# Optimization experiments

Measured on AMD Instinct MI355X. Metric: run time of the kernel, lower is better.

The kernel has to match this reference:

```python
import jax, jax.numpy as jnp
import numpy as np

LOCAL_RANGE = 7  # module default local_range
NUM_HEADS = 8


def setup_inputs() -> dict:
    key = jax.random.key(0)
    k1, k2, k3 = jax.random.split(key, 3)
    B, S, D = 2, 2048, 512
    hidden_states = jax.random.normal(k1, (B, S, D), dtype=jnp.float32)
    scale = 1.0 / (D ** 0.5)
    Wq = jax.random.normal(k2, (D, D), dtype=jnp.float32) * scale
    Wk = jax.random.normal(k3, (D, D), dtype=jnp.float32) * scale
    return {"hidden_states": hidden_states, "Wq": Wq, "Wk": Wk}


def reference(hidden_states, Wq, Wk):
    B, S, D = hidden_states.shape
    H = NUM_HEADS
    dh = D // H
    # inner attention: only attn_weights matter (context_layer is overwritten)
    q = (hidden_states @ Wq).reshape(B, S, H, dh).transpose(0, 2, 1, 3)  # [B,H,S,dh]
    k = (hidden_states @ Wk).reshape(B, S, H, dh).transpose(0, 2, 1, 3)  # [B,H,S,dh]
    scores = jnp.einsum('bhid,bhjd->bhij', q, k) / (dh ** 0.5)          # [B,H,S,S]
    attn_weights = jax.nn.softmax(scores, axis=-1)
    # band-diagonal local mask: |i-j| <= local_range (vectorized form of the python loop)
    idx = jnp.arange(S)
    band = (jnp.abs(idx[:, None] - idx[None, :]) <= LOCAL_RANGE).astype(attn_weights.dtype)  # [S,S]
    local_w = attn_weights * band
    local_w = local_w / (jnp.sum(local_w, axis=-1, keepdims=True) + 1e-6)
    # context = matmul(local_attn_weights, hidden_states): per-head contraction
    context = jnp.einsum('bhij,bjd->bhid', local_w, hidden_states)       # [B,H,S,D]
    return context
```

## Files before the change

kernel.cpp:

```cpp
#include <hip/hip_runtime.h>
#include <hip/hip_bf16.h>
#include <math.h>

#define SEQ   2048
#define DIM   512
#define NH    8
#define DH    64
#define LR    7

typedef __bf16 bf16_t;
typedef __bf16 bf16x8 __attribute__((ext_vector_type(8)));
typedef float  f32x4  __attribute__((ext_vector_type(4)));

typedef __attribute__((address_space(3))) void  lds_void;
typedef __attribute__((address_space(1))) const void gbl_cvoid;

__global__ __launch_bounds__(256) void prep(
    const float* __restrict__ hs,
    const float* __restrict__ Wq, const float* __restrict__ Wk,
    bf16_t* __restrict__ hsb,
    bf16_t* __restrict__ Wt)
{
    const int tid = threadIdx.x;
    const int bx  = blockIdx.x;

    if (bx < 1024) {
        const size_t base = ((size_t)bx * 256 + tid) * 8;
        const float4 f0 = *(const float4*)(hs + base);
        const float4 f1 = *(const float4*)(hs + base + 4);
        union { bf16_t b[8]; uint4 u; } cv;
        cv.b[0]=(bf16_t)f0.x; cv.b[1]=(bf16_t)f0.y; cv.b[2]=(bf16_t)f0.z; cv.b[3]=(bf16_t)f0.w;
        cv.b[4]=(bf16_t)f1.x; cv.b[5]=(bf16_t)f1.y; cv.b[6]=(bf16_t)f1.z; cv.b[7]=(bf16_t)f1.w;
        *(uint4*)(hsb + base) = cv.u;
        return;
    }

    __shared__ float tile[64][68];
    const int t  = bx - 1024;
    const int k0 = (t & 7) * 64;
    const int n0 = (t >> 3) * 64;
    const float* W = (n0 < DIM) ? Wq : Wk;
    const int nn0 = n0 & (DIM - 1);

    #pragma unroll
    for (int ph = 0; ph < 4; ++ph) {
        const int kk = ph * 16 + (tid >> 4);
        const int nn = (tid & 15) * 4;
        const float4 v = *(const float4*)(W + (size_t)(k0 + kk) * DIM + nn0 + nn);
        tile[kk][nn + 0] = v.x; tile[kk][nn + 1] = v.y;
        tile[kk][nn + 2] = v.z; tile[kk][nn + 3] = v.w;
    }
    __syncthreads();
    #pragma unroll
    for (int ph = 0; ph < 4; ++ph) {
        const int nn = ph * 16 + (tid >> 4);
        const int kk = (tid & 15) * 4;
        union { bf16_t b[4]; ushort4 u; } cv;
        #pragma unroll
        for (int u = 0; u < 4; ++u) cv.b[u] = (bf16_t)tile[kk + u][nn];
        *(ushort4*)(Wt + (size_t)(n0 + nn) * DIM + k0 + kk) = cv.u;
    }
}

__global__ __launch_bounds__(256) void qk_gemm_mfma(
    const bf16_t* __restrict__ A,
    const bf16_t* __restrict__ Bt,
    float* __restrict__ C)
{
    __shared__ bf16_t As[64][32];
    __shared__ bf16_t Bs[128][32];

    const int tid  = threadIdx.x;
    const int wave = tid >> 6;
    const int lane = tid & 63;
    const int l15  = lane & 15;
    const int quad = lane >> 4;
    const int wm   = (wave >> 1) * 32;
    const int wn   = (wave & 1) * 64;
    const int m0   = blockIdx.x * 64;
    const int n0   = blockIdx.y * 128;

    const int srow = lane >> 2;
    const int scol = (lane & 3) * 8;

    const bf16_t* agp = A  + (size_t)(m0 + wave * 16 + srow) * DIM + scol;
    const bf16_t* bgp = Bt + (size_t)(n0 + wave * 32 + srow) * DIM + scol;
    bf16_t* alp = &As[wave * 16][0];
    bf16_t* blp = &Bs[wave * 32][0];

    f32x4 acc[2][4] = {};

    for (int k0 = 0; k0 < DIM; k0 += 32) {
        __builtin_amdgcn_global_load_lds((gbl_cvoid*)(agp + k0),
                                         (lds_void*)alp, 16, 0, 0);
        __builtin_amdgcn_global_load_lds((gbl_cvoid*)(bgp + k0),
                                         (lds_void*)blp, 16, 0, 0);
        __builtin_amdgcn_global_load_lds((gbl_cvoid*)(bgp + 16 * DIM + k0),
                                         (lds_void*)(blp + 16 * 32), 16, 0, 0);
        __syncthreads();

        bf16x8 af[2], bfv[4];
        #pragma unroll
        for (int t = 0; t < 2; ++t)
            af[t] = *(const bf16x8*)&As[wm + t * 16 + l15][quad * 8];
        #pragma unroll
        for (int t = 0; t < 4; ++t)
            bfv[t] = *(const bf16x8*)&Bs[wn + t * 16 + l15][quad * 8];

        #pragma unroll
        for (int mi = 0; mi < 2; ++mi)
            #pragma unroll
            for (int ni = 0; ni < 4; ++ni)
                acc[mi][ni] = __builtin_amdgcn_mfma_f32_16x16x32_bf16(
                    af[mi], bfv[ni], acc[mi][ni], 0, 0, 0);
        __syncthreads();
    }

    #pragma unroll
    for (int mi = 0; mi < 2; ++mi) {
        #pragma unroll
        for (int ni = 0; ni < 4; ++ni) {
            const int col = n0 + wn + ni * 16 + l15;
            #pragma unroll
            for (int r = 0; r < 4; ++r) {
                const int row = m0 + wm + mi * 16 + quad * 4 + r;
                C[(size_t)row * 1024 + col] = acc[mi][ni][r];
            }
        }
    }
}

#define TI 8
#define NROW (TI + 2 * LR)

__global__ __launch_bounds__(256) void local_attn3(
    const float* __restrict__ hs,
    const float* __restrict__ qk,
    float* __restrict__ out)
{
    __shared__ float band[NROW][DIM + 4];
    __shared__ float qst[TI][DIM + 4];
    __shared__ float sw[NH * TI][16];
    __shared__ float wn[NH * TI][16];

    const int tid = threadIdx.x;
    const int i0  = blockIdx.x * TI;
    const int b   = blockIdx.y;

    {
        for (int idx = tid; idx < NROW * 128; idx += 256) {
            const int r  = idx >> 7;
            const int c4 = idx & 127;
            int jg = i0 - LR + r;
            jg = jg < 0 ? 0 : (jg > SEQ - 1 ? SEQ - 1 : jg);
            const float4 v = *(const float4*)(qk + (size_t)(b * SEQ + jg) * 1024 + DIM + c4 * 4);
            *(float4*)&band[r][c4 * 4] = v;
        }
        {
            const int r  = tid >> 5;
            const int c4 = (tid & 31) * 4;
            const float4* src = (const float4*)(qk + (size_t)(b * SEQ + i0 + r) * 1024) + c4;
            #pragma unroll
            for (int u = 0; u < 4; ++u)
                *(float4*)&qst[r][(c4 + u) * 4] = src[u];
        }
    }
    __syncthreads();

    {
        const int pair = tid >> 2;
        const int h  = pair >> 3;
        const int ii = pair & (TI - 1);
        const int jq = tid & 3;
        const int i  = i0 + ii;
        const float4* qp = (const float4*)&qst[ii][h * DH];
        #pragma unroll
        for (int jj = 0; jj < 4; ++jj) {
            const int j = jq * 4 + jj;
            if (j >= 15) break;
            const int jg = i - LR + j;
            float s = -1e30f;
            if (jg >= 0 && jg < SEQ) {
                const float4* kp = (const float4*)&band[ii + j][h * DH];
                float a = 0.f;
                #pragma unroll
                for (int u = 0; u < DH / 4; ++u) {
                    const float4 qv = qp[u];
                    const float4 kv = kp[u];
                    a += qv.x * kv.x + qv.y * kv.y + qv.z * kv.z + qv.w * kv.w;
                }
                s = a * 0.125f;
            }
            sw[pair][j] = s;
        }
    }
    __syncthreads();

    if (tid < NH * TI) {
        float v[15], m = -1e30f;
        #pragma unroll
        for (int j = 0; j < 15; ++j) { v[j] = sw[tid][j]; m = fmaxf(m, v[j]); }
        float sum = 0.f;
        #pragma unroll
        for (int j = 0; j < 15; ++j) { v[j] = __expf(v[j] - m); sum += v[j]; }
        const float inv = 1.f / sum;
        #pragma unroll
        for (int j = 0; j < 15; ++j) wn[tid][j] = v[j] * inv;
    }
    {
        for (int idx = tid; idx < NROW * 128; idx += 256) {
            const int r  = idx >> 7;
            const int c4 = idx & 127;
            int jg = i0 - LR + r;
            jg = jg < 0 ? 0 : (jg > SEQ - 1 ? SEQ - 1 : jg);
            const float4 v = *(const float4*)(hs + ((size_t)b * SEQ + jg) * DIM + c4 * 4);
            *(float4*)&band[r][c4 * 4] = v;
        }
    }
    __syncthreads();

    {
        const int h  = tid >> 5;
        const int iq = (tid >> 4) & 1;
        const int dg = tid & 15;

        float wreg[4][15];
        #pragma unroll
        for (int t = 0; t < 4; ++t) {
            const int pair = h * TI + iq * 4 + t;
            #pragma unroll
            for (int j = 0; j < 15; ++j) wreg[t][j] = wn[pair][j];
        }

        const int r0 = iq * 4;
        float* op = out + ((size_t)(b * NH + h) * SEQ + i0 + iq * 4) * DIM;

        for (int c = 0; c < DIM / 64; ++c) {
            const int dbase = c * 64 + dg * 4;
            float4 a0 = {0,0,0,0}, a1 = {0,0,0,0}, a2 = {0,0,0,0}, a3 = {0,0,0,0};
            #pragma unroll
            for (int rr = 0; rr < 18; ++rr) {
                const float4 v = *(const float4*)&band[r0 + rr][dbase];
                if (rr <= 14) {
                    const float w = wreg[0][rr];
                    a0.x += w * v.x; a0.y += w * v.y; a0.z += w * v.z; a0.w += w * v.w;
                }
                if (rr >= 1 && rr <= 15) {
                    const float w = wreg[1][rr - 1];
                    a1.x += w * v.x; a1.y += w * v.y; a1.z += w * v.z; a1.w += w * v.w;
                }
                if (rr >= 2 && rr <= 16) {
                    const float w = wreg[2][rr - 2];
                    a2.x += w * v.x; a2.y += w * v.y; a2.z += w * v.z; a2.w += w * v.w;
                }
                if (rr >= 3) {
                    const float w = wreg[3][rr - 3];
                    a3.x += w * v.x; a3.y += w * v.y; a3.z += w * v.z; a3.w += w * v.w;
                }
            }
            *(float4*)(op + (size_t)0 * DIM + dbase) = a0;
            *(float4*)(op + (size_t)1 * DIM + dbase) = a1;
            *(float4*)(op + (size_t)2 * DIM + dbase) = a2;
            *(float4*)(op + (size_t)3 * DIM + dbase) = a3;
        }
    }
}

extern "C" void kernel_launch(void* const* d_in, const int* in_sizes, int n_in,
                              void* d_out, int out_size, void* d_ws, size_t ws_size,
                              hipStream_t stream)
{
    const float* hs = (const float*)d_in[0];
    const float* Wq = (const float*)d_in[1];
    const float* Wk = (const float*)d_in[2];
    float* out = (float*)d_out;

    const int B = in_sizes[0] / (SEQ * DIM);
    const int M = B * SEQ;

    bf16_t* hsb = (bf16_t*)d_ws;
    bf16_t* Wt  = (bf16_t*)((char*)d_ws + (4 << 20));
    float*  qk  = (float*)((char*)d_ws + (5 << 20));

    prep<<<1024 + 128, 256, 0, stream>>>(hs, Wq, Wk, hsb, Wt);
    qk_gemm_mfma<<<dim3(M / 64, 1024 / 128), 256, 0, stream>>>(hsb, Wt, qk);
    local_attn3<<<dim3(SEQ / TI, B), 256, 0, stream>>>(hs, qk, out);
}
```

Measured before the change: 117.1 us.

## Store QK in bf16 and compute band scores with MFMA in local attention

The QK GEMM now writes its output in bf16 instead of fp32, which halves the intermediate traffic, and it loads K in steps of 64 using two LDS buffers per step. The local attention kernel pulls Q, K and the hidden-state band into a shared LDS union with async global_load_lds. It then computes the banded scores with 16x16x32 bf16 MFMAs instead of scalar fp32 dot products. This cuts memory traffic and score compute, but the bf16 rounding of Q and K lowers the precision of the scores.

```diff
diff --git a/kernel.cpp b/kernel.cpp
--- a/kernel.cpp
+++ b/kernel.cpp
@@ -7,6 +7,8 @@
 #define NH    8
 #define DH    64
 #define LR    7
+#define TI    8
+#define NROW  (TI + 2 * LR)
 
 typedef __bf16 bf16_t;
 typedef __bf16 bf16x8 __attribute__((ext_vector_type(8)));
@@ -65,10 +67,10 @@
 __global__ __launch_bounds__(256) void qk_gemm_mfma(
     const bf16_t* __restrict__ A,
     const bf16_t* __restrict__ Bt,
-    float* __restrict__ C)
-{
-    __shared__ bf16_t As[64][32];
-    __shared__ bf16_t Bs[128][32];
+    bf16_t* __restrict__ C)
+{
+    __shared__ bf16_t As0[64 * 32], As1[64 * 32];
+    __shared__ bf16_t Bs0[128 * 32], Bs1[128 * 32];
 
     const int tid  = threadIdx.x;
     const int wave = tid >> 6;
@@ -76,7 +78,7 @@
     const int l15  = lane & 15;
     const int quad = lane >> 4;
     const int wm   = (wave >> 1) * 32;
-    const int wn   = (wave & 1) * 64;
+    const int wn_  = (wave & 1) * 64;
     const int m0   = blockIdx.x * 64;
     const int n0   = blockIdx.y * 128;
 
@@ -85,34 +87,40 @@
 
     const bf16_t* agp = A  + (size_t)(m0 + wave * 16 + srow) * DIM + scol;
     const bf16_t* bgp = Bt + (size_t)(n0 + wave * 32 + srow) * DIM + scol;
-    bf16_t* alp = &As[wave * 16][0];
-    bf16_t* blp = &Bs[wave * 32][0];
+    bf16_t* al0 = As0 + wave * 16 * 32;
+    bf16_t* al1 = As1 + wave * 16 * 32;
+    bf16_t* bl0 = Bs0 + wave * 32 * 32;
+    bf16_t* bl1 = Bs1 + wave * 32 * 32;
 
     f32x4 acc[2][4] = {};
 
-    for (int k0 = 0; k0 < DIM; k0 += 32) {
-        __builtin_amdgcn_global_load_lds((gbl_cvoid*)(agp + k0),
-                                         (lds_void*)alp, 16, 0, 0);
-        __builtin_amdgcn_global_load_lds((gbl_cvoid*)(bgp + k0),
-                                         (lds_void*)blp, 16, 0, 0);
-        __builtin_amdgcn_global_load_lds((gbl_cvoid*)(bgp + 16 * DIM + k0),
-                                         (lds_void*)(blp + 16 * 32), 16, 0, 0);
+    for (int k0 = 0; k0 < DIM; k0 += 64) {
+        __builtin_amdgcn_global_load_lds((gbl_cvoid*)(agp + k0),      (lds_void*)al0, 16, 0, 0);
+        __builtin_amdgcn_global_load_lds((gbl_cvoid*)(agp + k0 + 32), (lds_void*)al1, 16, 0, 0);
+        __builtin_amdgcn_global_load_lds((gbl_cvoid*)(bgp + k0),      (lds_void*)bl0, 16, 0, 0);
+        __builtin_amdgcn_global_load_lds((gbl_cvoid*)(bgp + k0 + 32), (lds_void*)bl1, 16, 0, 0);
+        __builtin_amdgcn_global_load_lds((gbl_cvoid*)(bgp + 16 * DIM + k0),      (lds_void*)(bl0 + 16 * 32), 16, 0, 0);
+        __builtin_amdgcn_global_load_lds((gbl_cvoid*)(bgp + 16 * DIM + k0 + 32), (lds_void*)(bl1 + 16 * 32), 16, 0, 0);
         __syncthreads();
 
-        bf16x8 af[2], bfv[4];
-        #pragma unroll
-        for (int t = 0; t < 2; ++t)
-            af[t] = *(const bf16x8*)&As[wm + t * 16 + l15][quad * 8];
-        #pragma unroll
-        for (int t = 0; t < 4; ++t)
-            bfv[t] = *(const bf16x8*)&Bs[wn + t * 16 + l15][quad * 8];
-
-        #pragma unroll
-        for (int mi = 0; mi < 2; ++mi)
+        #pragma unroll
+        for (int s = 0; s < 2; ++s) {
+            const bf16_t* PA = s ? As1 : As0;
+            const bf16_t* PB = s ? Bs1 : Bs0;
+            bf16x8 af[2], bfv[4];
+            #pragma unroll
+            for (int mi = 0; mi < 2; ++mi)
+                af[mi] = *(const bf16x8*)(PA + (wm + mi * 16 + l15) * 32 + quad * 8);
             #pragma unroll
             for (int ni = 0; ni < 4; ++ni)
-                acc[mi][ni] = __builtin_amdgcn_mfma_f32_16x16x32_bf16(
-                    af[mi], bfv[ni], acc[mi][ni], 0, 0, 0);
+                bfv[ni] = *(const bf16x8*)(PB + (wn_ + ni * 16 + l15) * 32 + quad * 8);
+            #pragma unroll
+            for (int mi = 0; mi < 2; ++mi)
+                #pragma unroll
+                for (int ni = 0; ni < 4; ++ni)
+                    acc[mi][ni] = __builtin_amdgcn_mfma_f32_16x16x32_bf16(
+                        af[mi], bfv[ni], acc[mi][ni], 0, 0, 0);
+        }
         __syncthreads();
     }
 
@@ -120,102 +128,100 @@
     for (int mi = 0; mi < 2; ++mi) {
         #pragma unroll
         for (int ni = 0; ni < 4; ++ni) {
-            const int col = n0 + wn + ni * 16 + l15;
+            const int col = n0 + wn_ + ni * 16 + l15;
             #pragma unroll
             for (int r = 0; r < 4; ++r) {
                 const int row = m0 + wm + mi * 16 + quad * 4 + r;
-                C[(size_t)row * 1024 + col] = acc[mi][ni][r];
-            }
-        }
-    }
-}
-
-#define TI 8
-#define NROW (TI + 2 * LR)
-
-__global__ __launch_bounds__(256) void local_attn3(
+                C[(size_t)row * 1024 + col] = (bf16_t)acc[mi][ni][r];
+            }
+        }
+    }
+}
+
+__global__ __launch_bounds__(256) void local_attn4(
     const float* __restrict__ hs,
-    const float* __restrict__ qk,
+    const bf16_t* __restrict__ qkb,
     float* __restrict__ out)
 {
-    __shared__ float band[NROW][DIM + 4];
-    __shared__ float qst[TI][DIM + 4];
-    __shared__ float sw[NH * TI][16];
+    __shared__ __align__(16) char uni[49152];
+    bf16_t* Qb   = (bf16_t*)uni;
+    bf16_t* Kb   = (bf16_t*)(uni + 16384);
+    float*  band = (float*)uni;
+    __shared__ float sw2[NH][TI][24];
     __shared__ float wn[NH * TI][16];
 
-    const int tid = threadIdx.x;
-    const int i0  = blockIdx.x * TI;
-    const int b   = blockIdx.y;
-
-    {
-        for (int idx = tid; idx < NROW * 128; idx += 256) {
-            const int r  = idx >> 7;
-            const int c4 = idx & 127;
-            int jg = i0 - LR + r;
-            jg = jg < 0 ? 0 : (jg > SEQ - 1 ? SEQ - 1 : jg);
-            const float4 v = *(const float4*)(qk + (size_t)(b * SEQ + jg) * 1024 + DIM + c4 * 4);
-            *(float4*)&band[r][c4 * 4] = v;
-        }
-        {
-            const int r  = tid >> 5;
-            const int c4 = (tid & 31) * 4;
-            const float4* src = (const float4*)(qk + (size_t)(b * SEQ + i0 + r) * 1024) + c4;
-            #pragma unroll
-            for (int u = 0; u < 4; ++u)
-                *(float4*)&qst[r][(c4 + u) * 4] = src[u];
-        }
-    }
-    __syncthreads();
-
-    {
-        const int pair = tid >> 2;
-        const int h  = pair >> 3;
-        const int ii = pair & (TI - 1);
-        const int jq = tid & 3;
+    const int tid  = threadIdx.x;
+    const int wave = tid >> 6;
+    const int lane = tid & 63;
+    const int l15  = lane & 15;
+    const int quad = lane >> 4;
+    const int i0   = blockIdx.x * TI;
+    const int b    = blockIdx.y;
+
+    for (int r = wave; r < TI; r += 4) {
+        const bf16_t* g = qkb + (size_t)(b * SEQ + i0 + r) * 1024 + lane * 8;
+        __builtin_amdgcn_global_load_lds((gbl_cvoid*)g, (lds_void*)(Qb + r * DIM), 16, 0, 0);
+    }
+    for (int r = wave; r < NROW; r += 4) {
+        int jg = i0 - LR + r;
+        jg = jg < 0 ? 0 : (jg > SEQ - 1 ? SEQ - 1 : jg);
+        const bf16_t* g = qkb + (size_t)(b * SEQ + jg) * 1024 + DIM + lane * 8;
+        __builtin_amdgcn_global_load_lds((gbl_cvoid*)g, (lds_void*)(Kb + r * DIM), 16, 0, 0);
+    }
+    __syncthreads();
+
+    #pragma unroll
+    for (int hh = 0; hh < 2; ++hh) {
+        const int h = wave * 2 + hh;
+        f32x4 sacc[2] = {};
+        #pragma unroll
+        for (int s = 0; s < 2; ++s) {
+            const bf16x8 aq = *(const bf16x8*)(Qb + l15 * DIM + h * DH + s * 32 + quad * 8);
+            #pragma unroll
+            for (int t = 0; t < 2; ++t) {
+                const bf16x8 bk = *(const bf16x8*)(Kb + (t * 16 + l15) * DIM + h * DH + s * 32 + quad * 8);
+                sacc[t] = __builtin_amdgcn_mfma_f32_16x16x32_bf16(aq, bk, sacc[t], 0, 0, 0);
+            }
+        }
+        #pragma unroll
+        for (int t = 0; t < 2; ++t) {
+            const int jj = t * 16 + l15;
+            if (jj < NROW) {
+                #pragma unroll
+                for (int r = 0; r < 4; ++r) {
+                    const int ii = quad * 4 + r;
+                    if (ii < TI) sw2[h][ii][jj] = sacc[t][r] * 0.125f;
+                }
+            }
+        }
+    }
+    __syncthreads();
+
+    for (int r = wave; r < NROW; r += 4) {
+        int jg = i0 - LR + r;
+        jg = jg < 0 ? 0 : (jg > SEQ - 1 ? SEQ - 1 : jg);
+        const float* g0 = hs + ((size_t)b * SEQ + jg) * DIM + lane * 4;
+        __builtin_amdgcn_global_load_lds((gbl_cvoid*)g0,         (lds_void*)(band + r * DIM),       16, 0, 0);
+        __builtin_amdgcn_global_load_lds((gbl_cvoid*)(g0 + 256), (lds_void*)(band + r * DIM + 256), 16, 0, 0);
+    }
+
+    if (tid < NH * TI) {
+        const int h  = tid >> 3;
+        const int ii = tid & (TI - 1);
         const int i  = i0 + ii;
-        const float4* qp = (const float4*)&qst[ii][h * DH];
-        #pragma unroll
-        for (int jj = 0; jj < 4; ++jj) {
-            const int j = jq * 4 + jj;
-            if (j >= 15) break;
-            const int jg = i - LR + j;
-            float s = -1e30f;
-            if (jg >= 0 && jg < SEQ) {
-                const float4* kp = (const float4*)&band[ii + j][h * DH];
-                float a = 0.f;
-                #pragma unroll
-                for (int u = 0; u < DH / 4; ++u) {
-                    const float4 qv = qp[u];
-                    const float4 kv = kp[u];
-                    a += qv.x * kv.x + qv.y * kv.y + qv.z * kv.z + qv.w * kv.w;
-                }
-                s = a * 0.125f;
-            }
-            sw[pair][j] = s;
-        }
-    }
-    __syncthreads();
-
-    if (tid < NH * TI) {
         float v[15], m = -1e30f;
         #pragma unroll
-        for (int j = 0; j < 15; ++j) { v[j] = sw[tid][j]; m = fmaxf(m, v[j]); }
+        for (int t = 0; t < 15; ++t) {
+            const int jg = i - LR + t;
+            v[t] = (jg >= 0 && jg < SEQ) ? sw2[h][ii][ii + t] : -1e30f;
+            m = fmaxf(m, v[t]);
+        }
         float sum = 0.f;
         #pragma unroll
-        for (int j = 0; j < 15; ++j) { v[j] = __expf(v[j] - m); sum += v[j]; }
+        for (int t = 0; t < 15; ++t) { v[t] = __expf(v[t] - m); sum += v[t]; }
         const float inv = 1.f / sum;
         #pragma unroll
-        for (int j = 0; j < 15; ++j) wn[tid][j] = v[j] * inv;
-    }
-    {
-        for (int idx = tid; idx < NROW * 128; idx += 256) {
-            const int r  = idx >> 7;
-            const int c4 = idx & 127;
-            int jg = i0 - LR + r;
-            jg = jg < 0 ? 0 : (jg > SEQ - 1 ? SEQ - 1 : jg);
-            const float4 v = *(const float4*)(hs + ((size_t)b * SEQ + jg) * DIM + c4 * 4);
-            *(float4*)&band[r][c4 * 4] = v;
-        }
+        for (int t = 0; t < 15; ++t) wn[tid][t] = v[t] * inv;
     }
     __syncthreads();
 
@@ -240,7 +246,7 @@
             float4 a0 = {0,0,0,0}, a1 = {0,0,0,0}, a2 = {0,0,0,0}, a3 = {0,0,0,0};
             #pragma unroll
             for (int rr = 0; rr < 18; ++rr) {
-                const float4 v = *(const float4*)&band[r0 + rr][dbase];
+                const float4 v = *(const float4*)&band[(r0 + rr) * DIM + dbase];
                 if (rr <= 14) {
                     const float w = wreg[0][rr];
                     a0.x += w * v.x; a0.y += w * v.y; a0.z += w * v.z; a0.w += w * v.w;
@@ -280,9 +286,9 @@
 
     bf16_t* hsb = (bf16_t*)d_ws;
     bf16_t* Wt  = (bf16_t*)((char*)d_ws + (4 << 20));
-    float*  qk  = (float*)((char*)d_ws + (5 << 20));
+    bf16_t* qkb = (bf16_t*)((char*)d_ws + (5 << 20));
 
     prep<<<1024 + 128, 256, 0, stream>>>(hs, Wq, Wk, hsb, Wt);
-    qk_gemm_mfma<<<dim3(M / 64, 1024 / 128), 256, 0, stream>>>(hsb, Wt, qk);
-    local_attn3<<<dim3(SEQ / TI, B), 256, 0, stream>>>(hs, qk, out);
-}
+    qk_gemm_mfma<<<dim3(M / 64, 1024 / 128), 256, 0, stream>>>(hsb, Wt, qkb);
+    local_attn4<<<dim3(SEQ / TI, B), 256, 0, stream>>>(hs, qkb, out);
+}
```

Measured after the change: 105.4 us. -10.0%, faster.
